# Performance work log

Measured on AMD Instinct MI355X. Metric: run time of the kernel, lower is better.

## Reference

```python
import jax, jax.numpy as jnp
import numpy as np

TOP_K = 2

def setup_inputs() -> dict:
    key = jax.random.key(0)
    k1, k2, k3, k4, k5 = jax.random.split(key, 5)
    B, S, D, F, E = 8, 4096, 1024, 2048, 16
    return {
        "hidden_states": jax.random.normal(k1, (B, S, D), dtype=jnp.float32),
        "router_w": jax.random.normal(k2, (E, D), dtype=jnp.float32) * 0.02,
        "gate_w": jax.random.normal(k3, (E, D, F), dtype=jnp.float32) * 0.02,
        "up_w": jax.random.normal(k4, (E, D, F), dtype=jnp.float32) * 0.02,
        "down_w": jax.random.normal(k5, (E, F, D), dtype=jnp.float32) * 0.02,
    }


def reference(hidden_states, router_w, gate_w, up_w, down_w):
    B, S, D = hidden_states.shape
    E = router_w.shape[0]
    x = hidden_states.reshape(-1, D)  # [T, D]
    T = x.shape[0]

    router_logits = x @ router_w.T  # [T, E]
    probs = jax.nn.softmax(router_logits, axis=-1)
    top_w, top_i = jax.lax.top_k(probs, TOP_K)  # [T, k] (no re-normalization in Jamba)

    # dense combine weights: w[t, e] = top-k weight if expert e selected else 0
    cw = jnp.zeros((T, E), dtype=x.dtype).at[jnp.arange(T)[:, None], top_i].set(top_w)

    out = jnp.zeros_like(x)
    for e in range(E):  # fixed, small expert loop; each step is [T,D]x[D,F] GEMMs
        h = jax.nn.silu(x @ gate_w[e]) * (x @ up_w[e])  # [T, F]
        out = out + cw[:, e:e + 1] * (h @ down_w[e])     # [T, D]

    return out.reshape(B, S, D), router_logits
```

## Files before the change

### kernel.cpp

```cpp
#include <hip/hip_runtime.h>


#define T_ 32768
#define D_ 1024
#define F_ 2048
#define E_ 16
#define P_ 65536
#define MAXTILES 528

typedef __bf16 bf16x8 __attribute__((ext_vector_type(8)));
typedef float floatx4 __attribute__((ext_vector_type(4)));
typedef unsigned short bfu;

#define O_XB 0ull
#define O_WG 67108864ull
#define O_WU 134217728ull
#define O_WD 201326592ull
#define O_H  268435456ull
#define O_CW 536870912ull
#define O_EI 537133056ull
#define O_PM 537395200ull
#define O_MT 537657344ull

__device__ __forceinline__ unsigned short f2bf(float f) {
  unsigned int u = __float_as_uint(f);
  u = u + 0x7fffu + ((u >> 16) & 1u);
  return (unsigned short)(u >> 16);
}

__device__ __forceinline__ void gload16(const void* g, void* l) {
  __builtin_amdgcn_global_load_lds(
      (const __attribute__((address_space(1))) unsigned int*)g,
      (__attribute__((address_space(3))) unsigned int*)l, 16, 0, 0);
}

__global__ __launch_bounds__(256) void transpose_cast_kernel(
    const float* __restrict__ src, bfu* __restrict__ dst, int R, int C) {
  __shared__ float tile[64][65];
  const int e = blockIdx.z;
  const int r0 = blockIdx.y * 64, c0 = blockIdx.x * 64;
  const size_t base = (size_t)e * R * C;
  const int tid = threadIdx.x;
  const int rr = tid >> 4;
  const int cc = (tid & 15) * 4;
  const float* sp = src + base + (size_t)(r0 + rr) * C + (c0 + cc);
#pragma unroll
  for (int i = 0; i < 4; ++i) {
    float4 v = *(const float4*)(sp + (size_t)(i * 16) * C);
    tile[rr + i * 16][cc + 0] = v.x;
    tile[rr + i * 16][cc + 1] = v.y;
    tile[rr + i * 16][cc + 2] = v.z;
    tile[rr + i * 16][cc + 3] = v.w;
  }
  __syncthreads();
  const int oc = tid >> 2;
  const int sg = (tid & 3) * 16;
  union { bfu b[16]; uint4 q[2]; } u;
#pragma unroll
  for (int j = 0; j < 16; ++j) u.b[j] = f2bf(tile[sg + j][oc]);
  bfu* dp = dst + base + (size_t)(c0 + oc) * R + (r0 + sg);
  ((uint4*)dp)[0] = u.q[0];
  ((uint4*)dp)[1] = u.q[1];
}

__global__ __launch_bounds__(256) void router_kernel(
    const float* __restrict__ x, const float* __restrict__ rw,
    bfu* __restrict__ xb, float* __restrict__ logits,
    float* __restrict__ cw, int* __restrict__ eidx, int* __restrict__ meta) {
  __shared__ int hist[16];
  const int tid = threadIdx.x, lane = tid & 63, wave = tid >> 6;
  if (tid < 16) hist[tid] = 0;
  __syncthreads();

  for (int tk = 0; tk < 8; ++tk) {
    const int t = blockIdx.x * 32 + wave * 8 + tk;
    const float* xp = x + (size_t)t * D_ + lane * 16;
    float xv[16];
#pragma unroll
    for (int i = 0; i < 4; ++i) {
      float4 v = ((const float4*)xp)[i];
      xv[i * 4 + 0] = v.x; xv[i * 4 + 1] = v.y;
      xv[i * 4 + 2] = v.z; xv[i * 4 + 3] = v.w;
    }
    union { bfu b[16]; uint4 q[2]; } u;
#pragma unroll
    for (int i = 0; i < 16; ++i) u.b[i] = f2bf(xv[i]);
    uint4* xbp = (uint4*)(xb + (size_t)t * D_ + lane * 16);
    xbp[0] = u.q[0];
    xbp[1] = u.q[1];

    float l[16];
#pragma unroll
    for (int e = 0; e < 16; ++e) {
      const float* wp = rw + (size_t)e * D_ + lane * 16;
      float s = 0.f;
#pragma unroll
      for (int i = 0; i < 4; ++i) {
        float4 w = ((const float4*)wp)[i];
        s += xv[i * 4 + 0] * w.x + xv[i * 4 + 1] * w.y +
             xv[i * 4 + 2] * w.z + xv[i * 4 + 3] * w.w;
      }
#pragma unroll
      for (int off = 32; off; off >>= 1) s += __shfl_xor(s, off);
      l[e] = s;
    }
    float m = l[0];
#pragma unroll
    for (int e = 1; e < 16; ++e) m = fmaxf(m, l[e]);
    float p[16], sum = 0.f;
#pragma unroll
    for (int e = 0; e < 16; ++e) { p[e] = expf(l[e] - m); sum += p[e]; }
    int e0 = 0; float b0 = p[0];
#pragma unroll
    for (int e = 1; e < 16; ++e) if (p[e] > b0) { b0 = p[e]; e0 = e; }
    int e1 = -1; float b1 = -1.f;
#pragma unroll
    for (int e = 0; e < 16; ++e) if (e != e0 && p[e] > b1) { b1 = p[e]; e1 = e; }
    if (lane < 16) logits[(size_t)t * 16 + lane] = l[lane];
    if (lane == 0) {
      float inv = 1.f / sum;
      cw[t * 2 + 0] = b0 * inv;
      cw[t * 2 + 1] = b1 * inv;
      eidx[t * 2 + 0] = e0;
      eidx[t * 2 + 1] = e1;
      atomicAdd(&hist[e0], 1);
      atomicAdd(&hist[e1], 1);
    }
  }
  __syncthreads();
  if (tid < 16) atomicAdd(&meta[tid * 32], hist[tid]);
}

__global__ void scan_kernel(int* __restrict__ meta) {
  if (threadIdx.x != 0) return;
  int off = 0, nt = 0;
  for (int e = 0; e < 16; ++e) {
    meta[1024 + e] = off;
    int n = meta[e * 32];
    for (int r = 0; r < n; r += 128) {
      meta[1056 + nt] = e;
      meta[1600 + nt] = off + r;
      ++nt;
    }
    off += n;
  }
  meta[1040] = off;
  meta[1041] = nt;
}

__global__ __launch_bounds__(256) void perm_kernel(
    const int* __restrict__ eidx, int* __restrict__ meta, int* __restrict__ perm) {
  __shared__ int wcnt[4][16];
  __shared__ int bbase[16];
  const int tid = threadIdx.x, lane = tid & 63, wave = tid >> 6;
  const int p = blockIdx.x * 256 + tid;
  const int e = eidx[p];
  const unsigned long long lt = (lane == 63) ? ~0ull >> 1
                                             : (1ull << lane) - 1;
  int rank = 0;
#pragma unroll
  for (int q = 0; q < 16; ++q) {
    unsigned long long m = __ballot(e == q);
    if (e == q) rank = __popcll(m & lt);
    if (lane == 0) wcnt[wave][q] = __popcll(m);
  }
  __syncthreads();
  if (tid < 16) {
    int s = 0;
#pragma unroll
    for (int w = 0; w < 4; ++w) { int c = wcnt[w][tid]; wcnt[w][tid] = s; s += c; }
    bbase[tid] = atomicAdd(&meta[512 + tid * 32], s);
  }
  __syncthreads();
  perm[meta[1024 + e] + bbase[e] + wcnt[wave][e] + rank] = p;
}

__global__ __launch_bounds__(256, 2) void gateup_kernel(
    const bfu* __restrict__ xb, const bfu* __restrict__ wg,
    const bfu* __restrict__ wu, bfu* __restrict__ h,
    const int* __restrict__ perm, const int* __restrict__ meta) {
  __shared__ bfu As[128 * 32];
  __shared__ bfu Bg[128 * 32];
  __shared__ bfu Bu[128 * 32];
  __shared__ int rowtok[128];

  const int tile = blockIdx.y;
  if (tile >= meta[1041]) return;
  const int e = meta[1056 + tile];
  const int row0 = meta[1600 + tile];
  const int nvalid = meta[1025 + e] - row0;
  const int n0 = blockIdx.x * 128;
  const int tid = threadIdx.x, lane = tid & 63, wave = tid >> 6;

  if (tid < 128) {
    int r = tid < nvalid ? tid : (nvalid - 1);
    rowtok[tid] = perm[row0 + r] >> 1;
  }
  __syncthreads();

  const int ldr = wave * 32 + (lane >> 2);
  const int kseg = (lane & 3) * 8;
  const bfu* ap1 = xb + (size_t)rowtok[ldr] * D_ + kseg;
  const bfu* ap2 = xb + (size_t)rowtok[ldr + 16] * D_ + kseg;
  const size_t wb = (size_t)e * F_ * D_;
  const bfu* gp1 = wg + wb + (size_t)(n0 + ldr) * D_ + kseg;
  const bfu* gp2 = gp1 + (size_t)16 * D_;
  const bfu* up1 = wu + wb + (size_t)(n0 + ldr) * D_ + kseg;
  const bfu* up2 = up1 + (size_t)16 * D_;
  bfu* al1 = As + (wave * 32) * 32;
  bfu* al2 = As + (wave * 32 + 16) * 32;
  bfu* gl1 = Bg + (wave * 32) * 32;
  bfu* gl2 = Bg + (wave * 32 + 16) * 32;
  bfu* ul1 = Bu + (wave * 32) * 32;
  bfu* ul2 = Bu + (wave * 32 + 16) * 32;

  const int wm = (wave >> 1) * 64, wn = (wave & 1) * 64;
  const int fro = (lane & 15) * 32 + (lane >> 4) * 8;
  const bf16x8* afp = (const bf16x8*)(As + wm * 32 + fro);
  const bf16x8* bgp = (const bf16x8*)(Bg + wn * 32 + fro);
  const bf16x8* bup = (const bf16x8*)(Bu + wn * 32 + fro);

  floatx4 accg[4][4] = {};
  floatx4 accu[4][4] = {};

  for (int k0 = 0; k0 < D_; k0 += 32) {
    gload16(ap1 + k0, al1);
    gload16(ap2 + k0, al2);
    gload16(gp1 + k0, gl1);
    gload16(gp2 + k0, gl2);
    gload16(up1 + k0, ul1);
    gload16(up2 + k0, ul2);
    __syncthreads();
    bf16x8 af[4], bgf[4], buf_[4];
#pragma unroll
    for (int i = 0; i < 4; ++i) {
      af[i] = afp[i * 64];
      bgf[i] = bgp[i * 64];
      buf_[i] = bup[i * 64];
    }
#pragma unroll
    for (int mi = 0; mi < 4; ++mi)
#pragma unroll
      for (int ni = 0; ni < 4; ++ni) {
        accg[mi][ni] = __builtin_amdgcn_mfma_f32_16x16x32_bf16(
            af[mi], bgf[ni], accg[mi][ni], 0, 0, 0);
        accu[mi][ni] = __builtin_amdgcn_mfma_f32_16x16x32_bf16(
            af[mi], buf_[ni], accu[mi][ni], 0, 0, 0);
      }
    __syncthreads();
  }

  bfu* slab = As + wave * 1024;
  const int sq = lane >> 4, sc = lane & 15;
  const int orow = lane >> 2, osg = (lane & 3) * 16;
#pragma unroll
  for (int mi = 0; mi < 4; ++mi) {
    __syncthreads();
#pragma unroll
    for (int ni = 0; ni < 4; ++ni) {
      floatx4 g = accg[mi][ni], v = accu[mi][ni];
#pragma unroll
      for (int i = 0; i < 4; ++i) {
        float gv = g[i];
        float hv = (gv / (1.f + __expf(-gv))) * v[i];
        slab[(sq * 4 + i) * 64 + ni * 16 + sc] = f2bf(hv);
      }
    }
    __syncthreads();
    const int prow = wm + mi * 16 + orow;
    if (prow < nvalid) {
      bfu* hp = h + (size_t)(row0 + prow) * F_ + (n0 + wn + osg);
      uint4 q0 = *(const uint4*)(slab + orow * 64 + osg);
      uint4 q1 = *(const uint4*)(slab + orow * 64 + osg + 8);
      ((uint4*)hp)[0] = q0;
      ((uint4*)hp)[1] = q1;
    }
  }
}

__global__ __launch_bounds__(256, 2) void down_kernel(
    const bfu* __restrict__ h, const bfu* __restrict__ wd,
    float* __restrict__ out, const float* __restrict__ cw,
    const int* __restrict__ perm, const int* __restrict__ meta) {
  __shared__ bfu As[128 * 32];
  __shared__ bfu Bs[128 * 32];
  __shared__ int rtok[128];
  __shared__ float rwt[128];

  const int tile = blockIdx.y;
  if (tile >= meta[1041]) return;
  const int e = meta[1056 + tile];
  const int row0 = meta[1600 + tile];
  const int nvalid = meta[1025 + e] - row0;
  const int n0 = blockIdx.x * 128;
  const int tid = threadIdx.x, lane = tid & 63, wave = tid >> 6;

  if (tid < 128) {
    if (tid < nvalid) {
      int pr = perm[row0 + tid];
      rtok[tid] = pr >> 1;
      rwt[tid] = cw[pr];
    } else {
      rtok[tid] = 0;
      rwt[tid] = 0.f;
    }
  }
  __syncthreads();

  const int ldr = wave * 32 + (lane >> 2);
  const int kseg = (lane & 3) * 8;
  const int r1 = min(ldr, nvalid - 1);
  const int r2 = min(ldr + 16, nvalid - 1);
  const bfu* ap1 = h + (size_t)(row0 + r1) * F_ + kseg;
  const bfu* ap2 = h + (size_t)(row0 + r2) * F_ + kseg;
  const bfu* bp1 = wd + (size_t)e * D_ * F_ + (size_t)(n0 + ldr) * F_ + kseg;
  const bfu* bp2 = bp1 + (size_t)16 * F_;
  bfu* al1 = As + (wave * 32) * 32;
  bfu* al2 = As + (wave * 32 + 16) * 32;
  bfu* bl1 = Bs + (wave * 32) * 32;
  bfu* bl2 = Bs + (wave * 32 + 16) * 32;

  const int wm = (wave >> 1) * 64, wn = (wave & 1) * 64;
  const int fro = (lane & 15) * 32 + (lane >> 4) * 8;
  const bf16x8* afp = (const bf16x8*)(As + wm * 32 + fro);
  const bf16x8* bfp = (const bf16x8*)(Bs + wn * 32 + fro);

  floatx4 acc[4][4] = {};
  for (int k0 = 0; k0 < F_; k0 += 32) {
    gload16(ap1 + k0, al1);
    gload16(ap2 + k0, al2);
    gload16(bp1 + k0, bl1);
    gload16(bp2 + k0, bl2);
    __syncthreads();
    bf16x8 af[4], bf_[4];
#pragma unroll
    for (int i = 0; i < 4; ++i) { af[i] = afp[i * 64]; bf_[i] = bfp[i * 64]; }
#pragma unroll
    for (int mi = 0; mi < 4; ++mi)
#pragma unroll
      for (int ni = 0; ni < 4; ++ni)
        acc[mi][ni] = __builtin_amdgcn_mfma_f32_16x16x32_bf16(
            af[mi], bf_[ni], acc[mi][ni], 0, 0, 0);
    __syncthreads();
  }

  const int sq = lane >> 4, sc = lane & 15;
#pragma unroll
  for (int mi = 0; mi < 4; ++mi) {
#pragma unroll
    for (int i = 0; i < 4; ++i) {
      const int r = wm + mi * 16 + sq * 4 + i;
      const float w = rwt[r];
      if (w != 0.f) {
        const int tok = rtok[r];
        float* op = out + (size_t)tok * D_ + n0 + wn + sc;
#pragma unroll
        for (int ni = 0; ni < 4; ++ni)
          atomicAdd(op + ni * 16, w * acc[mi][ni][i]);
      }
    }
  }
}

extern "C" void kernel_launch(void* const* d_in, const int* in_sizes, int n_in,
                              void* d_out, int out_size, void* d_ws, size_t ws_size,
                              hipStream_t stream) {
  const float* x  = (const float*)d_in[0];
  const float* rw = (const float*)d_in[1];
  const float* gw = (const float*)d_in[2];
  const float* uw = (const float*)d_in[3];
  const float* dw = (const float*)d_in[4];
  float* out = (float*)d_out;
  float* logits = out + (size_t)T_ * D_;

  char* ws = (char*)d_ws;
  bfu* xb  = (bfu*)(ws + O_XB);
  bfu* wgt = (bfu*)(ws + O_WG);
  bfu* wut = (bfu*)(ws + O_WU);
  bfu* wdt = (bfu*)(ws + O_WD);
  bfu* hb  = (bfu*)(ws + O_H);
  float* cwp = (float*)(ws + O_CW);
  int* eip  = (int*)(ws + O_EI);
  int* perm = (int*)(ws + O_PM);
  int* meta = (int*)(ws + O_MT);

  hipMemsetAsync(out, 0, (size_t)T_ * D_ * sizeof(float), stream);
  hipMemsetAsync(meta, 0, 4096, stream);

  transpose_cast_kernel<<<dim3(F_ / 64, D_ / 64, E_), 256, 0, stream>>>(gw, wgt, D_, F_);
  transpose_cast_kernel<<<dim3(F_ / 64, D_ / 64, E_), 256, 0, stream>>>(uw, wut, D_, F_);
  transpose_cast_kernel<<<dim3(D_ / 64, F_ / 64, E_), 256, 0, stream>>>(dw, wdt, F_, D_);

  router_kernel<<<T_ / 32, 256, 0, stream>>>(x, rw, xb, logits, cwp, eip, meta);
  scan_kernel<<<1, 64, 0, stream>>>(meta);
  perm_kernel<<<P_ / 256, 256, 0, stream>>>(eip, meta, perm);

  gateup_kernel<<<dim3(F_ / 128, MAXTILES), 256, 0, stream>>>(xb, wgt, wut, hb, perm, meta);
  down_kernel<<<dim3(D_ / 128, MAXTILES), 256, 0, stream>>>(hb, wdt, out, cwp, perm, meta);
}
```

Before: 1.820 ms.

## Pipeline expert GEMMs with 4-stage LDS ring, swizzle, and 256-row tiles

Rewrites the gate/up and down grouped GEMM kernels to use 512-thread blocks covering 256-row tiles (every other 128-row tile is skipped), a 4-slot shared-memory ring with three tiles of global-load prefetch, and XOR-swizzled LDS layout to avoid bank conflicts. Manual s_waitcnt, barriers, sched_barrier and setprio interleave loads with MFMA work instead of fully syncing each k-step. The goal is to hide global-load latency and raise MFMA utilization. The cost is much larger LDS per block and reliance on the tile metadata being aligned to 128-row boundaries per expert.

```diff
diff --git a/kernel.cpp b/kernel.cpp
--- a/kernel.cpp
+++ b/kernel.cpp
@@ -175,87 +175,120 @@
   perm[meta[1024 + e] + bbase[e] + wcnt[wave][e] + rank] = p;
 }
 
-__global__ __launch_bounds__(256, 2) void gateup_kernel(
+__global__ __launch_bounds__(512, 2) void gateup_kernel(
     const bfu* __restrict__ xb, const bfu* __restrict__ wg,
     const bfu* __restrict__ wu, bfu* __restrict__ h,
     const int* __restrict__ perm, const int* __restrict__ meta) {
-  __shared__ bfu As[128 * 32];
-  __shared__ bfu Bg[128 * 32];
-  __shared__ bfu Bu[128 * 32];
-  __shared__ int rowtok[128];
+  __shared__ bfu sA[4][8192];
+  __shared__ bfu sG[4][4096];
+  __shared__ bfu sU[4][4096];
+  __shared__ int rowtok[256];
 
   const int tile = blockIdx.y;
   if (tile >= meta[1041]) return;
   const int e = meta[1056 + tile];
   const int row0 = meta[1600 + tile];
+  if ((row0 - meta[1024 + e]) & 128) return;
   const int nvalid = meta[1025 + e] - row0;
   const int n0 = blockIdx.x * 128;
   const int tid = threadIdx.x, lane = tid & 63, wave = tid >> 6;
-
-  if (tid < 128) {
+  const int wm = wave >> 1, wn = wave & 1;
+
+  if (tid < 256) {
     int r = tid < nvalid ? tid : (nvalid - 1);
     rowtok[tid] = perm[row0 + r] >> 1;
   }
   __syncthreads();
 
-  const int ldr = wave * 32 + (lane >> 2);
-  const int kseg = (lane & 3) * 8;
-  const bfu* ap1 = xb + (size_t)rowtok[ldr] * D_ + kseg;
-  const bfu* ap2 = xb + (size_t)rowtok[ldr + 16] * D_ + kseg;
-  const size_t wb = (size_t)e * F_ * D_;
-  const bfu* gp1 = wg + wb + (size_t)(n0 + ldr) * D_ + kseg;
-  const bfu* gp2 = gp1 + (size_t)16 * D_;
-  const bfu* up1 = wu + wb + (size_t)(n0 + ldr) * D_ + kseg;
-  const bfu* up2 = up1 + (size_t)16 * D_;
-  bfu* al1 = As + (wave * 32) * 32;
-  bfu* al2 = As + (wave * 32 + 16) * 32;
-  bfu* gl1 = Bg + (wave * 32) * 32;
-  bfu* gl2 = Bg + (wave * 32 + 16) * 32;
-  bfu* ul1 = Bu + (wave * 32) * 32;
-  bfu* ul2 = Bu + (wave * 32 + 16) * 32;
-
-  const int wm = (wave >> 1) * 64, wn = (wave & 1) * 64;
-  const int fro = (lane & 15) * 32 + (lane >> 4) * 8;
-  const bf16x8* afp = (const bf16x8*)(As + wm * 32 + fro);
-  const bf16x8* bgp = (const bf16x8*)(Bg + wn * 32 + fro);
-  const bf16x8* bup = (const bf16x8*)(Bu + wn * 32 + fro);
+  const int srow = wave * 16 + (lane >> 2);
+  const int kx = ((lane & 3) ^ ((srow >> 1) & 3)) << 3;
+  const bfu* aSrc0 = xb + (size_t)rowtok[srow] * D_ + kx;
+  const bfu* aSrc1 = xb + (size_t)rowtok[srow + 128] * D_ + kx;
+  const size_t wbase = (size_t)e * F_ * D_;
+  const bfu* gSrc = wg + wbase + (size_t)(n0 + srow) * D_ + kx;
+  const bfu* uSrc = wu + wbase + (size_t)(n0 + srow) * D_ + kx;
+  const int dA0 = wave * 512;
+  const int dA1 = 4096 + wave * 512;
+  const int dB  = wave * 512;
+
+  const int kg = lane >> 4;
+  int offA[4], offB[4];
+#pragma unroll
+  for (int i = 0; i < 4; ++i) {
+    const int row = wm * 64 + i * 16 + (lane & 15);
+    offA[i] = row * 32 + ((kg ^ ((row >> 1) & 3)) << 3);
+    const int col = wn * 64 + i * 16 + (lane & 15);
+    offB[i] = col * 32 + ((kg ^ ((col >> 1) & 3)) << 3);
+  }
 
   floatx4 accg[4][4] = {};
   floatx4 accu[4][4] = {};
 
-  for (int k0 = 0; k0 < D_; k0 += 32) {
-    gload16(ap1 + k0, al1);
-    gload16(ap2 + k0, al2);
-    gload16(gp1 + k0, gl1);
-    gload16(gp2 + k0, gl2);
-    gload16(up1 + k0, ul1);
-    gload16(up2 + k0, ul2);
-    __syncthreads();
-    bf16x8 af[4], bgf[4], buf_[4];
-#pragma unroll
-    for (int i = 0; i < 4; ++i) {
-      af[i] = afp[i * 64];
-      bgf[i] = bgp[i * 64];
-      buf_[i] = bup[i * 64];
-    }
+#pragma unroll
+  for (int pt = 0; pt < 3; ++pt) {
+    const int ko = pt * 32;
+    gload16(aSrc0 + ko, &sA[pt][dA0]);
+    gload16(aSrc1 + ko, &sA[pt][dA1]);
+    gload16(gSrc + ko, &sG[pt][dB]);
+    gload16(uSrc + ko, &sU[pt][dB]);
+  }
+  asm volatile("s_waitcnt vmcnt(8)" ::: "memory");
+  __builtin_amdgcn_s_barrier();
+
+#pragma unroll 4
+  for (int kt = 0; kt < 32; ++kt) {
+    const int slot = kt & 3;
+    bf16x8 af[4], bg[4], bu[4];
+    if (kt < 29) {
+      const int s2 = (kt + 3) & 3, ko = (kt + 3) * 32;
+      gload16(aSrc0 + ko, &sA[s2][dA0]);
+      gload16(aSrc1 + ko, &sA[s2][dA1]);
+    }
+#pragma unroll
+    for (int i = 0; i < 4; ++i) af[i] = *(const bf16x8*)&sA[slot][offA[i]];
+#pragma unroll
+    for (int i = 0; i < 4; ++i) bg[i] = *(const bf16x8*)&sG[slot][offB[i]];
+    __builtin_amdgcn_s_barrier();
+    asm volatile("s_waitcnt lgkmcnt(0)" ::: "memory");
+    __builtin_amdgcn_sched_barrier(0);
+    __builtin_amdgcn_s_setprio(1);
 #pragma unroll
     for (int mi = 0; mi < 4; ++mi)
 #pragma unroll
-      for (int ni = 0; ni < 4; ++ni) {
+      for (int ni = 0; ni < 4; ++ni)
         accg[mi][ni] = __builtin_amdgcn_mfma_f32_16x16x32_bf16(
-            af[mi], bgf[ni], accg[mi][ni], 0, 0, 0);
+            af[mi], bg[ni], accg[mi][ni], 0, 0, 0);
+    __builtin_amdgcn_s_setprio(0);
+    __builtin_amdgcn_s_barrier();
+    if (kt < 29) {
+      const int s2 = (kt + 3) & 3, ko = (kt + 3) * 32;
+      gload16(gSrc + ko, &sG[s2][dB]);
+      gload16(uSrc + ko, &sU[s2][dB]);
+    }
+#pragma unroll
+    for (int i = 0; i < 4; ++i) bu[i] = *(const bf16x8*)&sU[slot][offB[i]];
+    __builtin_amdgcn_s_barrier();
+    asm volatile("s_waitcnt lgkmcnt(0)" ::: "memory");
+    __builtin_amdgcn_sched_barrier(0);
+    __builtin_amdgcn_s_setprio(1);
+#pragma unroll
+    for (int mi = 0; mi < 4; ++mi)
+#pragma unroll
+      for (int ni = 0; ni < 4; ++ni)
         accu[mi][ni] = __builtin_amdgcn_mfma_f32_16x16x32_bf16(
-            af[mi], buf_[ni], accu[mi][ni], 0, 0, 0);
-      }
-    __syncthreads();
-  }
-
-  bfu* slab = As + wave * 1024;
+            af[mi], bu[ni], accu[mi][ni], 0, 0, 0);
+    __builtin_amdgcn_s_setprio(0);
+    if (kt < 29)       asm volatile("s_waitcnt vmcnt(8)" ::: "memory");
+    else if (kt == 29) asm volatile("s_waitcnt vmcnt(4)" ::: "memory");
+    else if (kt == 30) asm volatile("s_waitcnt vmcnt(0)" ::: "memory");
+    __builtin_amdgcn_s_barrier();
+  }
+
+  bfu* slab = &sA[0][0] + wave * 1024;
   const int sq = lane >> 4, sc = lane & 15;
   const int orow = lane >> 2, osg = (lane & 3) * 16;
 #pragma unroll
   for (int mi = 0; mi < 4; ++mi) {
-    __syncthreads();
 #pragma unroll
     for (int ni = 0; ni < 4; ++ni) {
       floatx4 g = accg[mi][ni], v = accu[mi][ni];
@@ -266,10 +299,9 @@
         slab[(sq * 4 + i) * 64 + ni * 16 + sc] = f2bf(hv);
       }
     }
-    __syncthreads();
-    const int prow = wm + mi * 16 + orow;
+    const int prow = wm * 64 + mi * 16 + orow;
     if (prow < nvalid) {
-      bfu* hp = h + (size_t)(row0 + prow) * F_ + (n0 + wn + osg);
+      bfu* hp = h + (size_t)(row0 + prow) * F_ + (n0 + wn * 64 + osg);
       uint4 q0 = *(const uint4*)(slab + orow * 64 + osg);
       uint4 q1 = *(const uint4*)(slab + orow * 64 + osg + 8);
       ((uint4*)hp)[0] = q0;
@@ -278,24 +310,26 @@
   }
 }
 
-__global__ __launch_bounds__(256, 2) void down_kernel(
+__global__ __launch_bounds__(512, 2) void down_kernel(
     const bfu* __restrict__ h, const bfu* __restrict__ wd,
     float* __restrict__ out, const float* __restrict__ cw,
     const int* __restrict__ perm, const int* __restrict__ meta) {
-  __shared__ bfu As[128 * 32];
-  __shared__ bfu Bs[128 * 32];
-  __shared__ int rtok[128];
-  __shared__ float rwt[128];
+  __shared__ bfu sA[4][8192];
+  __shared__ bfu sB[4][4096];
+  __shared__ int rtok[256];
+  __shared__ float rwt[256];
 
   const int tile = blockIdx.y;
   if (tile >= meta[1041]) return;
   const int e = meta[1056 + tile];
   const int row0 = meta[1600 + tile];
+  if ((row0 - meta[1024 + e]) & 128) return;
   const int nvalid = meta[1025 + e] - row0;
   const int n0 = blockIdx.x * 128;
   const int tid = threadIdx.x, lane = tid & 63, wave = tid >> 6;
-
-  if (tid < 128) {
+  const int wm = wave >> 1, wn = wave & 1;
+
+  if (tid < 256) {
     if (tid < nvalid) {
       int pr = perm[row0 + tid];
       rtok[tid] = pr >> 1;
@@ -307,41 +341,66 @@
   }
   __syncthreads();
 
-  const int ldr = wave * 32 + (lane >> 2);
-  const int kseg = (lane & 3) * 8;
-  const int r1 = min(ldr, nvalid - 1);
-  const int r2 = min(ldr + 16, nvalid - 1);
-  const bfu* ap1 = h + (size_t)(row0 + r1) * F_ + kseg;
-  const bfu* ap2 = h + (size_t)(row0 + r2) * F_ + kseg;
-  const bfu* bp1 = wd + (size_t)e * D_ * F_ + (size_t)(n0 + ldr) * F_ + kseg;
-  const bfu* bp2 = bp1 + (size_t)16 * F_;
-  bfu* al1 = As + (wave * 32) * 32;
-  bfu* al2 = As + (wave * 32 + 16) * 32;
-  bfu* bl1 = Bs + (wave * 32) * 32;
-  bfu* bl2 = Bs + (wave * 32 + 16) * 32;
-
-  const int wm = (wave >> 1) * 64, wn = (wave & 1) * 64;
-  const int fro = (lane & 15) * 32 + (lane >> 4) * 8;
-  const bf16x8* afp = (const bf16x8*)(As + wm * 32 + fro);
-  const bf16x8* bfp = (const bf16x8*)(Bs + wn * 32 + fro);
+  const int srow = wave * 16 + (lane >> 2);
+  const int kx = ((lane & 3) ^ ((srow >> 1) & 3)) << 3;
+  const int ra = srow < nvalid ? srow : nvalid - 1;
+  const int rb = (srow + 128) < nvalid ? (srow + 128) : nvalid - 1;
+  const bfu* aSrc0 = h + (size_t)(row0 + ra) * F_ + kx;
+  const bfu* aSrc1 = h + (size_t)(row0 + rb) * F_ + kx;
+  const bfu* bSrc = wd + (size_t)e * D_ * F_ + (size_t)(n0 + srow) * F_ + kx;
+  const int dA0 = wave * 512, dA1 = 4096 + wave * 512, dB = wave * 512;
+
+  const int kg = lane >> 4;
+  int offA[4], offB[4];
+#pragma unroll
+  for (int i = 0; i < 4; ++i) {
+    const int row = wm * 64 + i * 16 + (lane & 15);
+    offA[i] = row * 32 + ((kg ^ ((row >> 1) & 3)) << 3);
+    const int col = wn * 64 + i * 16 + (lane & 15);
+    offB[i] = col * 32 + ((kg ^ ((col >> 1) & 3)) << 3);
+  }
 
   floatx4 acc[4][4] = {};
-  for (int k0 = 0; k0 < F_; k0 += 32) {
-    gload16(ap1 + k0, al1);
-    gload16(ap2 + k0, al2);
-    gload16(bp1 + k0, bl1);
-    gload16(bp2 + k0, bl2);
-    __syncthreads();
+
+#pragma unroll
+  for (int pt = 0; pt < 3; ++pt) {
+    const int ko = pt * 32;
+    gload16(aSrc0 + ko, &sA[pt][dA0]);
+    gload16(aSrc1 + ko, &sA[pt][dA1]);
+    gload16(bSrc + ko, &sB[pt][dB]);
+  }
+  asm volatile("s_waitcnt vmcnt(6)" ::: "memory");
+  __builtin_amdgcn_s_barrier();
+
+#pragma unroll 4
+  for (int kt = 0; kt < 64; ++kt) {
+    const int slot = kt & 3;
+    if (kt < 61) {
+      const int s2 = (kt + 3) & 3, ko = (kt + 3) * 32;
+      gload16(aSrc0 + ko, &sA[s2][dA0]);
+      gload16(aSrc1 + ko, &sA[s2][dA1]);
+      gload16(bSrc + ko, &sB[s2][dB]);
+    }
     bf16x8 af[4], bf_[4];
 #pragma unroll
-    for (int i = 0; i < 4; ++i) { af[i] = afp[i * 64]; bf_[i] = bfp[i * 64]; }
+    for (int i = 0; i < 4; ++i) af[i] = *(const bf16x8*)&sA[slot][offA[i]];
+#pragma unroll
+    for (int i = 0; i < 4; ++i) bf_[i] = *(const bf16x8*)&sB[slot][offB[i]];
+    __builtin_amdgcn_s_barrier();
+    asm volatile("s_waitcnt lgkmcnt(0)" ::: "memory");
+    __builtin_amdgcn_sched_barrier(0);
+    __builtin_amdgcn_s_setprio(1);
 #pragma unroll
     for (int mi = 0; mi < 4; ++mi)
 #pragma unroll
       for (int ni = 0; ni < 4; ++ni)
         acc[mi][ni] = __builtin_amdgcn_mfma_f32_16x16x32_bf16(
             af[mi], bf_[ni], acc[mi][ni], 0, 0, 0);
-    __syncthreads();
+    __builtin_amdgcn_s_setprio(0);
+    if (kt < 61)       asm volatile("s_waitcnt vmcnt(6)" ::: "memory");
+    else if (kt == 61) asm volatile("s_waitcnt vmcnt(3)" ::: "memory");
+    else if (kt == 62) asm volatile("s_waitcnt vmcnt(0)" ::: "memory");
+    __builtin_amdgcn_s_barrier();
   }
 
   const int sq = lane >> 4, sc = lane & 15;
@@ -349,11 +408,11 @@
   for (int mi = 0; mi < 4; ++mi) {
 #pragma unroll
     for (int i = 0; i < 4; ++i) {
-      const int r = wm + mi * 16 + sq * 4 + i;
+      const int r = wm * 64 + mi * 16 + sq * 4 + i;
       const float w = rwt[r];
       if (w != 0.f) {
         const int tok = rtok[r];
-        float* op = out + (size_t)tok * D_ + n0 + wn + sc;
+        float* op = out + (size_t)tok * D_ + n0 + wn * 64 + sc;
 #pragma unroll
         for (int ni = 0; ni < 4; ++ni)
           atomicAdd(op + ni * 16, w * acc[mi][ni][i]);
@@ -395,6 +454,6 @@
   scan_kernel<<<1, 64, 0, stream>>>(meta);
   perm_kernel<<<P_ / 256, 256, 0, stream>>>(eip, meta, perm);
 
-  gateup_kernel<<<dim3(F_ / 128, MAXTILES), 256, 0, stream>>>(xb, wgt, wut, hb, perm, meta);
-  down_kernel<<<dim3(D_ / 128, MAXTILES), 256, 0, stream>>>(hb, wdt, out, cwp, perm, meta);
-}
+  gateup_kernel<<<dim3(F_ / 128, MAXTILES), 512, 0, stream>>>(xb, wgt, wut, hb, perm, meta);
+  down_kernel<<<dim3(D_ / 128, MAXTILES), 512, 0, stream>>>(hb, wdt, out, cwp, perm, meta);
+}
```

Result: slower. 2.893 ms (+58.9%).

## Double K-tile depth, XOR-swizzle LDS layout, and remap workgroups across XCDs

Applied to the files above, without the earlier changes.

Both expert GEMM kernels now stage 64-wide K slices per iteration instead of 32, halving the number of barrier pairs per tile. The LDS tile uses an XOR swizzle on 16-byte segments, both in the direct global-to-LDS loads and in the fragment reads, to avoid bank conflicts. Workgroup IDs are remapped so consecutive tiles land on the same XCD, which is meant to improve L2 reuse of expert weights. The cost is doubled shared memory per block, which may limit occupancy with the gate/up kernel's three buffers.

```diff
diff --git a/kernel.cpp b/kernel.cpp
--- a/kernel.cpp
+++ b/kernel.cpp
@@ -179,17 +179,22 @@
     const bfu* __restrict__ xb, const bfu* __restrict__ wg,
     const bfu* __restrict__ wu, bfu* __restrict__ h,
     const int* __restrict__ perm, const int* __restrict__ meta) {
-  __shared__ bfu As[128 * 32];
-  __shared__ bfu Bg[128 * 32];
-  __shared__ bfu Bu[128 * 32];
+  __shared__ bfu As[128 * 64];
+  __shared__ bfu Bg[128 * 64];
+  __shared__ bfu Bu[128 * 64];
   __shared__ int rowtok[128];
 
-  const int tile = blockIdx.y;
+  const int GX = F_ / 128;
+  const int NWG = GX * MAXTILES;
+  const int d = blockIdx.y * GX + blockIdx.x;
+  const int wgi = (d & 7) * (NWG >> 3) + (d >> 3);
+  const int tile = wgi / GX;
+  const int n0 = (wgi % GX) * 128;
+
   if (tile >= meta[1041]) return;
   const int e = meta[1056 + tile];
   const int row0 = meta[1600 + tile];
   const int nvalid = meta[1025 + e] - row0;
-  const int n0 = blockIdx.x * 128;
   const int tid = threadIdx.x, lane = tid & 63, wave = tid >> 6;
 
   if (tid < 128) {
@@ -198,55 +203,59 @@
   }
   __syncthreads();
 
-  const int ldr = wave * 32 + (lane >> 2);
-  const int kseg = (lane & 3) * 8;
-  const bfu* ap1 = xb + (size_t)rowtok[ldr] * D_ + kseg;
-  const bfu* ap2 = xb + (size_t)rowtok[ldr + 16] * D_ + kseg;
-  const size_t wb = (size_t)e * F_ * D_;
-  const bfu* gp1 = wg + wb + (size_t)(n0 + ldr) * D_ + kseg;
-  const bfu* gp2 = gp1 + (size_t)16 * D_;
-  const bfu* up1 = wu + wb + (size_t)(n0 + ldr) * D_ + kseg;
-  const bfu* up2 = up1 + (size_t)16 * D_;
-  bfu* al1 = As + (wave * 32) * 32;
-  bfu* al2 = As + (wave * 32 + 16) * 32;
-  bfu* gl1 = Bg + (wave * 32) * 32;
-  bfu* gl2 = Bg + (wave * 32 + 16) * 32;
-  bfu* ul1 = Bu + (wave * 32) * 32;
-  bfu* ul2 = Bu + (wave * 32 + 16) * 32;
+  const int sr = wave * 8 + (lane >> 3);
+  const int kx = ((lane & 7) ^ (lane >> 3)) << 3;
+  const size_t wbase = (size_t)e * F_ * D_;
+  const bfu* aP[4]; const bfu* gP[4]; const bfu* uP[4];
+#pragma unroll
+  for (int j = 0; j < 4; ++j) {
+    const int row = j * 32 + sr;
+    aP[j] = xb + (size_t)rowtok[row] * D_ + kx;
+    gP[j] = wg + wbase + (size_t)(n0 + row) * D_ + kx;
+    uP[j] = wu + wbase + (size_t)(n0 + row) * D_ + kx;
+  }
 
   const int wm = (wave >> 1) * 64, wn = (wave & 1) * 64;
-  const int fro = (lane & 15) * 32 + (lane >> 4) * 8;
-  const bf16x8* afp = (const bf16x8*)(As + wm * 32 + fro);
-  const bf16x8* bgp = (const bf16x8*)(Bg + wn * 32 + fro);
-  const bf16x8* bup = (const bf16x8*)(Bu + wn * 32 + fro);
+  const int rb = lane & 15, kseg = lane >> 4, x7 = rb & 7;
+  int offA[4], offB[4];
+#pragma unroll
+  for (int i = 0; i < 4; ++i) {
+    offA[i] = (wm + i * 16 + rb) * 64 + ((kseg ^ x7) << 3);
+    offB[i] = (wn + i * 16 + rb) * 64 + ((kseg ^ x7) << 3);
+  }
 
   floatx4 accg[4][4] = {};
   floatx4 accu[4][4] = {};
 
-  for (int k0 = 0; k0 < D_; k0 += 32) {
-    gload16(ap1 + k0, al1);
-    gload16(ap2 + k0, al2);
-    gload16(gp1 + k0, gl1);
-    gload16(gp2 + k0, gl2);
-    gload16(up1 + k0, ul1);
-    gload16(up2 + k0, ul2);
-    __syncthreads();
-    bf16x8 af[4], bgf[4], buf_[4];
-#pragma unroll
-    for (int i = 0; i < 4; ++i) {
-      af[i] = afp[i * 64];
-      bgf[i] = bgp[i * 64];
-      buf_[i] = bup[i * 64];
-    }
-#pragma unroll
-    for (int mi = 0; mi < 4; ++mi)
-#pragma unroll
-      for (int ni = 0; ni < 4; ++ni) {
-        accg[mi][ni] = __builtin_amdgcn_mfma_f32_16x16x32_bf16(
-            af[mi], bgf[ni], accg[mi][ni], 0, 0, 0);
-        accu[mi][ni] = __builtin_amdgcn_mfma_f32_16x16x32_bf16(
-            af[mi], buf_[ni], accu[mi][ni], 0, 0, 0);
+  for (int k0 = 0; k0 < D_; k0 += 64) {
+#pragma unroll
+    for (int j = 0; j < 4; ++j) {
+      const int db = (j * 32 + wave * 8) * 64;
+      gload16(aP[j] + k0, As + db);
+      gload16(gP[j] + k0, Bg + db);
+      gload16(uP[j] + k0, Bu + db);
+    }
+    __syncthreads();
+#pragma unroll
+    for (int kh = 0; kh < 2; ++kh) {
+      const int kf = kh << 5;
+      bf16x8 af[4], bg[4], bu[4];
+#pragma unroll
+      for (int i = 0; i < 4; ++i) {
+        af[i] = *(const bf16x8*)&As[offA[i] ^ kf];
+        bg[i] = *(const bf16x8*)&Bg[offB[i] ^ kf];
+        bu[i] = *(const bf16x8*)&Bu[offB[i] ^ kf];
       }
+#pragma unroll
+      for (int mi = 0; mi < 4; ++mi)
+#pragma unroll
+        for (int ni = 0; ni < 4; ++ni) {
+          accg[mi][ni] = __builtin_amdgcn_mfma_f32_16x16x32_bf16(
+              af[mi], bg[ni], accg[mi][ni], 0, 0, 0);
+          accu[mi][ni] = __builtin_amdgcn_mfma_f32_16x16x32_bf16(
+              af[mi], bu[ni], accu[mi][ni], 0, 0, 0);
+        }
+    }
     __syncthreads();
   }
 
@@ -282,17 +291,22 @@
     const bfu* __restrict__ h, const bfu* __restrict__ wd,
     float* __restrict__ out, const float* __restrict__ cw,
     const int* __restrict__ perm, const int* __restrict__ meta) {
-  __shared__ bfu As[128 * 32];
-  __shared__ bfu Bs[128 * 32];
+  __shared__ bfu As[128 * 64];
+  __shared__ bfu Bs[128 * 64];
   __shared__ int rtok[128];
   __shared__ float rwt[128];
 
-  const int tile = blockIdx.y;
+  const int GX = D_ / 128;
+  const int NWG = GX * MAXTILES;
+  const int d = blockIdx.y * GX + blockIdx.x;
+  const int wgi = (d & 7) * (NWG >> 3) + (d >> 3);
+  const int tile = wgi / GX;
+  const int n0 = (wgi % GX) * 128;
+
   if (tile >= meta[1041]) return;
   const int e = meta[1056 + tile];
   const int row0 = meta[1600 + tile];
   const int nvalid = meta[1025 + e] - row0;
-  const int n0 = blockIdx.x * 128;
   const int tid = threadIdx.x, lane = tid & 63, wave = tid >> 6;
 
   if (tid < 128) {
@@ -307,40 +321,52 @@
   }
   __syncthreads();
 
-  const int ldr = wave * 32 + (lane >> 2);
-  const int kseg = (lane & 3) * 8;
-  const int r1 = min(ldr, nvalid - 1);
-  const int r2 = min(ldr + 16, nvalid - 1);
-  const bfu* ap1 = h + (size_t)(row0 + r1) * F_ + kseg;
-  const bfu* ap2 = h + (size_t)(row0 + r2) * F_ + kseg;
-  const bfu* bp1 = wd + (size_t)e * D_ * F_ + (size_t)(n0 + ldr) * F_ + kseg;
-  const bfu* bp2 = bp1 + (size_t)16 * F_;
-  bfu* al1 = As + (wave * 32) * 32;
-  bfu* al2 = As + (wave * 32 + 16) * 32;
-  bfu* bl1 = Bs + (wave * 32) * 32;
-  bfu* bl2 = Bs + (wave * 32 + 16) * 32;
+  const int sr = wave * 8 + (lane >> 3);
+  const int kx = ((lane & 7) ^ (lane >> 3)) << 3;
+  const bfu* aP[4]; const bfu* bP[4];
+#pragma unroll
+  for (int j = 0; j < 4; ++j) {
+    const int row = j * 32 + sr;
+    const int ar = row < nvalid ? row : (nvalid - 1);
+    aP[j] = h + (size_t)(row0 + ar) * F_ + kx;
+    bP[j] = wd + (size_t)e * D_ * F_ + (size_t)(n0 + row) * F_ + kx;
+  }
 
   const int wm = (wave >> 1) * 64, wn = (wave & 1) * 64;
-  const int fro = (lane & 15) * 32 + (lane >> 4) * 8;
-  const bf16x8* afp = (const bf16x8*)(As + wm * 32 + fro);
-  const bf16x8* bfp = (const bf16x8*)(Bs + wn * 32 + fro);
+  const int rb = lane & 15, kseg = lane >> 4, x7 = rb & 7;
+  int offA[4], offB[4];
+#pragma unroll
+  for (int i = 0; i < 4; ++i) {
+    offA[i] = (wm + i * 16 + rb) * 64 + ((kseg ^ x7) << 3);
+    offB[i] = (wn + i * 16 + rb) * 64 + ((kseg ^ x7) << 3);
+  }
 
   floatx4 acc[4][4] = {};
-  for (int k0 = 0; k0 < F_; k0 += 32) {
-    gload16(ap1 + k0, al1);
-    gload16(ap2 + k0, al2);
-    gload16(bp1 + k0, bl1);
-    gload16(bp2 + k0, bl2);
-    __syncthreads();
-    bf16x8 af[4], bf_[4];
-#pragma unroll
-    for (int i = 0; i < 4; ++i) { af[i] = afp[i * 64]; bf_[i] = bfp[i * 64]; }
-#pragma unroll
-    for (int mi = 0; mi < 4; ++mi)
-#pragma unroll
-      for (int ni = 0; ni < 4; ++ni)
-        acc[mi][ni] = __builtin_amdgcn_mfma_f32_16x16x32_bf16(
-            af[mi], bf_[ni], acc[mi][ni], 0, 0, 0);
+
+  for (int k0 = 0; k0 < F_; k0 += 64) {
+#pragma unroll
+    for (int j = 0; j < 4; ++j) {
+      const int db = (j * 32 + wave * 8) * 64;
+      gload16(aP[j] + k0, As + db);
+      gload16(bP[j] + k0, Bs + db);
+    }
+    __syncthreads();
+#pragma unroll
+    for (int kh = 0; kh < 2; ++kh) {
+      const int kf = kh << 5;
+      bf16x8 af[4], bf_[4];
+#pragma unroll
+      for (int i = 0; i < 4; ++i) {
+        af[i] = *(const bf16x8*)&As[offA[i] ^ kf];
+        bf_[i] = *(const bf16x8*)&Bs[offB[i] ^ kf];
+      }
+#pragma unroll
+      for (int mi = 0; mi < 4; ++mi)
+#pragma unroll
+        for (int ni = 0; ni < 4; ++ni)
+          acc[mi][ni] = __builtin_amdgcn_mfma_f32_16x16x32_bf16(
+              af[mi], bf_[ni], acc[mi][ni], 0, 0, 0);
+    }
     __syncthreads();
   }
 
```

New measurement: 1.618 ms. -11.1%, faster.
